# Performance work log

Hardware: AMD Instinct MI355X
Metric: run time of the kernel (lower is better)

## Reference

```python
import jax, jax.numpy as jnp
import numpy as np

N = 8192
F_IN = 256
F_OUT = 64
ALPHA = 0.2  # leaky relu negative slope
MASK_VAL = -9e15


def setup_inputs() -> dict:
    key = jax.random.key(0)
    k1, k2, k3, k4, k5, k6 = jax.random.split(key, 6)
    stdv_lin = 1.0 / np.sqrt(F_IN)
    stdv_a = 1.0 / np.sqrt(2 * F_OUT)
    return {
        "input": jax.random.normal(k1, (N, F_IN), dtype=jnp.float32),
        "adj": jax.random.randint(k2, (N, N), 0, 2, dtype=jnp.int32),
        "W": jax.random.uniform(k3, (F_IN, F_OUT), minval=-stdv_lin, maxval=stdv_lin, dtype=jnp.float32),
        "b_lin": jax.random.uniform(k4, (F_OUT,), minval=-stdv_lin, maxval=stdv_lin, dtype=jnp.float32),
        "a": jax.random.uniform(k5, (2 * F_OUT, 1), minval=-stdv_a, maxval=stdv_a, dtype=jnp.float32),
        "bias": jax.random.uniform(k6, (F_OUT,), minval=-stdv_a, maxval=stdv_a, dtype=jnp.float32),
    }


def reference(input, adj, W, b_lin, a, bias):
    # h = Linear(input): [N, F_OUT]
    h = input @ W + b_lin
    # e[i,j] = leaky_relu(a1 . h_i + a2 . h_j)  (equivalent to the repeat/cat/matmul in torch,
    # without materializing the [N, N, 2*F_OUT] tensor)
    a1 = a[:F_OUT, 0]
    a2 = a[F_OUT:, 0]
    s1 = h @ a1  # [N]
    s2 = h @ a2  # [N]
    e = jax.nn.leaky_relu(s1[:, None] + s2[None, :], negative_slope=ALPHA)  # [N, N]
    attention = jnp.where(adj > 0, e, MASK_VAL)
    attention = jax.nn.softmax(attention, axis=1)
    # dropout is identity in eval mode (training=False)
    output = attention @ h + bias
    return output
```

## Files before the change

### kernel.cpp

```cpp
#include <hip/hip_runtime.h>

#define N 8192
#define FIN 256
#define FOUT 64
#define ALPHA 0.2f

typedef float f32x4 __attribute__((ext_vector_type(4)));
typedef short s16x4 __attribute__((ext_vector_type(4)));

static __device__ __forceinline__ unsigned short f2bf(float x) {
    unsigned u = __float_as_uint(x);
    u += 0x7fffu + ((u >> 16) & 1u);
    return (unsigned short)(u >> 16);
}

__global__ __launch_bounds__(256) void k_linear(
    const float* __restrict__ input, const float* __restrict__ W,
    const float* __restrict__ b_lin, const float* __restrict__ a,
    unsigned short* __restrict__ hT, float* __restrict__ s1, float* __restrict__ s2)
{
    __shared__ float in_sh[32 * FIN];
    __shared__ float hst[64][33];
    int t = threadIdx.x;
    int i0 = blockIdx.x * 32;

    const float4* gin = (const float4*)(input + (size_t)i0 * FIN);
    float4* lin = (float4*)in_sh;
#pragma unroll
    for (int m = 0; m < 8; m++) lin[m * 256 + t] = gin[m * 256 + t];

    int f = t & 63, g = t >> 6;
    float a1v = a[f], a2v = a[FOUT + f], blv = b_lin[f];
    __syncthreads();

    float h[8];
#pragma unroll
    for (int r = 0; r < 8; r++) h[r] = blv;
#pragma unroll 4
    for (int k = 0; k < FIN; k++) {
        float wv = W[k * FOUT + f];
#pragma unroll
        for (int r = 0; r < 8; r++) h[r] += in_sh[(g * 8 + r) * FIN + k] * wv;
    }

#pragma unroll
    for (int r = 0; r < 8; r++) {
        hst[f][g * 8 + r] = h[r];
        float v1 = h[r] * a1v, v2 = h[r] * a2v;
#pragma unroll
        for (int d = 1; d < 64; d <<= 1) { v1 += __shfl_xor(v1, d); v2 += __shfl_xor(v2, d); }
        if (f == 0) { s1[i0 + g * 8 + r] = v1; s2[i0 + g * 8 + r] = v2; }
    }
    __syncthreads();

    int fo = t >> 2, seg = t & 3;
    unsigned pk[4];
#pragma unroll
    for (int m = 0; m < 4; m++) {
        unsigned lo = f2bf(hst[fo][seg * 8 + 2 * m]);
        unsigned hi = f2bf(hst[fo][seg * 8 + 2 * m + 1]);
        pk[m] = lo | (hi << 16);
    }
    int4 v; v.x = (int)pk[0]; v.y = (int)pk[1]; v.z = (int)pk[2]; v.w = (int)pk[3];
    *(int4*)(hT + (size_t)fo * N + i0 + seg * 8) = v;
}

__global__ __launch_bounds__(256) void k_s2max(const float* __restrict__ s2,
                                               float* __restrict__ s2max)
{
    __shared__ float red[4];
    int t = threadIdx.x;
    float m = -1e30f;
    for (int k = t; k < N; k += 256) m = fmaxf(m, s2[k]);
#pragma unroll
    for (int d = 1; d < 64; d <<= 1) m = fmaxf(m, __shfl_xor(m, d));
    if ((t & 63) == 0) red[t >> 6] = m;
    __syncthreads();
    if (t == 0) s2max[0] = fmaxf(fmaxf(red[0], red[1]), fmaxf(red[2], red[3]));
}

__global__ __launch_bounds__(256) void k_attn(
    const int* __restrict__ adj, const float* __restrict__ s1g,
    const float* __restrict__ s2g, const unsigned short* __restrict__ hT,
    const float* __restrict__ s2maxp, const float* __restrict__ bias,
    float* __restrict__ numP, float* __restrict__ denP, float* __restrict__ out,
    int log2c)
{
    extern __shared__ char smem[];
    unsigned short* tile = (unsigned short*)smem;
    int clen = N >> log2c;
    float* s2sh = (float*)(smem + 9216);
    float* densh = (float*)(smem + 9216 + (clen << 2));

    const float LOG2E = 1.4426950408889634f;
    int bid = blockIdx.x;
    int chunk = bid & ((1 << log2c) - 1);
    int rb = bid >> log2c;
    int jstart = chunk * clen;
    int t = threadIdx.x, w = t >> 6, l = t & 63;
    int l15 = l & 15, kg = l >> 4;

    for (int idx = t; idx < (clen >> 2); idx += 256)
        ((float4*)s2sh)[idx] = ((const float4*)(s2g + jstart))[idx];

    int i0 = rb * 64;
    int i = i0 + w * 16 + l15;
    float s1v = s1g[i];
    float s2m = s2maxp[0];
    float mx = s1v + s2m; mx = fmaxf(mx, ALPHA * mx);
    float m2 = mx * LOG2E;

    f32x4 acc[4] = {};
    float dacc = 0.f;
    const int4* adjrow = (const int4*)(adj + (size_t)i * N);
    __syncthreads();

    int iters = clen >> 6;
    for (int it = 0; it < iters; it++) {
        int j0 = it * 64;
#pragma unroll
        for (int m = 0; m < 2; m++) {
            int c = t + m * 256;
            int fr = c >> 3, off = (c & 7) * 8;
            *(int4*)(tile + fr * 72 + off) =
                *(const int4*)(hT + (size_t)fr * N + jstart + j0 + off);
        }
        s16x4 afr[4];
#pragma unroll
        for (int kb = 0; kb < 4; kb++) {
            int jloc = j0 + kb * 16 + kg * 4;
            int4 av = adjrow[(jstart + jloc) >> 2];
            float4 sv = *(const float4*)&s2sh[jloc];
            float p0, p1, p2, p3;
            { float x = s1v + sv.x; x = fmaxf(x, ALPHA * x); p0 = (av.x > 0) ? exp2f(x * LOG2E - m2) : 0.f; }
            { float x = s1v + sv.y; x = fmaxf(x, ALPHA * x); p1 = (av.y > 0) ? exp2f(x * LOG2E - m2) : 0.f; }
            { float x = s1v + sv.z; x = fmaxf(x, ALPHA * x); p2 = (av.z > 0) ? exp2f(x * LOG2E - m2) : 0.f; }
            { float x = s1v + sv.w; x = fmaxf(x, ALPHA * x); p3 = (av.w > 0) ? exp2f(x * LOG2E - m2) : 0.f; }
            dacc += (p0 + p1) + (p2 + p3);
            s16x4 af;
            af[0] = (short)f2bf(p0); af[1] = (short)f2bf(p1);
            af[2] = (short)f2bf(p2); af[3] = (short)f2bf(p3);
            afr[kb] = af;
        }
        __syncthreads();
#pragma unroll
        for (int nt = 0; nt < 4; nt++) {
#pragma unroll
            for (int kb = 0; kb < 4; kb++) {
                s16x4 bfr = *(const s16x4*)(tile + (nt * 16 + l15) * 72 + kb * 16 + kg * 4);
                acc[nt] = __builtin_amdgcn_mfma_f32_16x16x16bf16_1k(afr[kb], bfr, acc[nt], 0, 0, 0);
            }
        }
        __syncthreads();
    }

    dacc += __shfl_xor(dacc, 16);
    dacc += __shfl_xor(dacc, 32);

    if (log2c == 0) {
        if (l < 16) densh[w * 16 + l] = dacc;
        __syncthreads();
#pragma unroll
        for (int nt = 0; nt < 4; nt++) {
#pragma unroll
            for (int r = 0; r < 4; r++) {
                int orow = w * 16 + kg * 4 + r;
                out[(size_t)(i0 + orow) * FOUT + nt * 16 + l15] =
                    acc[nt][r] / densh[orow] + bias[nt * 16 + l15];
            }
        }
    } else {
        if (l < 16) denP[(size_t)chunk * N + i0 + w * 16 + l] = dacc;
#pragma unroll
        for (int nt = 0; nt < 4; nt++) {
#pragma unroll
            for (int r = 0; r < 4; r++) {
                int orow = w * 16 + kg * 4 + r;
                numP[((size_t)chunk * N + i0 + orow) * FOUT + nt * 16 + l15] = acc[nt][r];
            }
        }
    }
}

__global__ __launch_bounds__(256) void k_finalize(
    const float* __restrict__ numP, const float* __restrict__ denP,
    const float* __restrict__ bias, float* __restrict__ out, int chunks)
{
    int idx = blockIdx.x * 256 + threadIdx.x;
    int i = idx >> 6, f = idx & 63;
    float nsum = 0.f, dsum = 0.f;
    for (int c = 0; c < chunks; c++) {
        nsum += numP[(size_t)c * (N * FOUT) + idx];
        dsum += denP[(size_t)c * N + i];
    }
    out[idx] = nsum / dsum + bias[f];
}

extern "C" void kernel_launch(void* const* d_in, const int* in_sizes, int n_in,
                              void* d_out, int out_size, void* d_ws, size_t ws_size,
                              hipStream_t stream)
{
    const float* input = (const float*)d_in[0];
    const int*   adj   = (const int*)d_in[1];
    const float* W     = (const float*)d_in[2];
    const float* b_lin = (const float*)d_in[3];
    const float* a     = (const float*)d_in[4];
    const float* bias  = (const float*)d_in[5];
    float* out = (float*)d_out;

    char* ws = (char*)d_ws;
    unsigned short* hT = (unsigned short*)ws;
    float* s1    = (float*)(ws + 1048576);
    float* s2    = (float*)(ws + 1048576 + 32768);
    float* s2max = (float*)(ws + 1048576 + 65536);
    size_t fixed = 1048576 + 65536 + 256;

    int log2c = 3;
    while (log2c > 0) {
        size_t need = (((size_t)N * FOUT + N) * 4u) << log2c;
        if (fixed + need <= ws_size) break;
        log2c--;
    }
    float* numP = (float*)(ws + fixed);
    float* denP = (float*)(ws + fixed + (((size_t)N * FOUT * 4) << log2c));

    hipLaunchKernelGGL(k_linear, dim3(256), dim3(256), 0, stream,
                       input, W, b_lin, a, hT, s1, s2);
    hipLaunchKernelGGL(k_s2max, dim3(1), dim3(256), 0, stream, s2, s2max);

    int clen = N >> log2c;
    size_t smem = 9216 + ((size_t)clen << 2) + 256;
    hipLaunchKernelGGL(k_attn, dim3(128 << log2c), dim3(256), smem, stream,
                       adj, s1, s2, hT, s2max, bias, numP, denP, out, log2c);
    if (log2c > 0)
        hipLaunchKernelGGL(k_finalize, dim3(2048), dim3(256), 0, stream,
                           numP, denP, bias, out, 1 << log2c);
}
```

Measured before the change: 94.73 us.

## Pre-swizzle h into MFMA fragment layout, prefetch adj, fuse s2 max via atomics

The linear kernel now writes h in a blocked bf16 layout that matches the MFMA B-fragment order. The attention kernel can then load B operands straight from global memory, with no LDS tile staging and no __syncthreads per iteration. Adjacency rows are register double-buffered so the next tile's loads are issued before the current exp/MFMA work. The separate s2-max kernel is replaced by an order-preserving atomicMax inside k_linear, which now runs smaller 16-row blocks, with a memset to initialise the key. The cost is more global and L2 traffic for B fragments, which each wave re-reads, and higher register pressure from the prefetch buffers.

Measured after the change: 129.3 us. 1.36x slower.

```diff
diff --git a/kernel.cpp b/kernel.cpp
--- a/kernel.cpp
+++ b/kernel.cpp
@@ -17,80 +17,76 @@
 __global__ __launch_bounds__(256) void k_linear(
     const float* __restrict__ input, const float* __restrict__ W,
     const float* __restrict__ b_lin, const float* __restrict__ a,
-    unsigned short* __restrict__ hT, float* __restrict__ s1, float* __restrict__ s2)
-{
-    __shared__ float in_sh[32 * FIN];
-    __shared__ float hst[64][33];
-    int t = threadIdx.x;
-    int i0 = blockIdx.x * 32;
-
-    const float4* gin = (const float4*)(input + (size_t)i0 * FIN);
-    float4* lin = (float4*)in_sh;
-#pragma unroll
-    for (int m = 0; m < 8; m++) lin[m * 256 + t] = gin[m * 256 + t];
-
-    int f = t & 63, g = t >> 6;
-    float a1v = a[f], a2v = a[FOUT + f], blv = b_lin[f];
+    unsigned short* __restrict__ hTf, float* __restrict__ s1, float* __restrict__ s2,
+    unsigned* __restrict__ s2max_enc)
+{
+    __shared__ float in_sh[16 * FIN];
+    __shared__ float hst[64][17];
+    int t = threadIdx.x, w = t >> 6, f = t & 63;
+    int i0 = blockIdx.x * 16;
+
+#pragma unroll
+    for (int r = 0; r < 4; r++) {
+        int row = w * 4 + r;
+        *(float4*)&in_sh[row * FIN + f * 4] =
+            *(const float4*)(input + (size_t)(i0 + row) * FIN + f * 4);
+    }
+
+    float a1v = a[f], a2v = a[FOUT + f];
+    float h[4];
+#pragma unroll
+    for (int r = 0; r < 4; r++) h[r] = b_lin[f];
+
+    for (int k4 = 0; k4 < FIN / 4; k4++) {
+        float wv0 = W[(k4 * 4 + 0) * FOUT + f];
+        float wv1 = W[(k4 * 4 + 1) * FOUT + f];
+        float wv2 = W[(k4 * 4 + 2) * FOUT + f];
+        float wv3 = W[(k4 * 4 + 3) * FOUT + f];
+#pragma unroll
+        for (int r = 0; r < 4; r++) {
+            float4 iv = *(const float4*)&in_sh[(w * 4 + r) * FIN + k4 * 4];
+            h[r] = fmaf(iv.x, wv0, h[r]);
+            h[r] = fmaf(iv.y, wv1, h[r]);
+            h[r] = fmaf(iv.z, wv2, h[r]);
+            h[r] = fmaf(iv.w, wv3, h[r]);
+        }
+    }
+
+    float wmax = -1e30f;
+#pragma unroll
+    for (int r = 0; r < 4; r++) {
+        hst[f][w * 4 + r] = h[r];
+        float v1 = h[r] * a1v, v2 = h[r] * a2v;
+#pragma unroll
+        for (int d = 1; d < 64; d <<= 1) { v1 += __shfl_xor(v1, d); v2 += __shfl_xor(v2, d); }
+        wmax = fmaxf(wmax, v2);
+        if (f == 0) { s1[i0 + w * 4 + r] = v1; s2[i0 + w * 4 + r] = v2; }
+    }
+    if (f == 0) {
+        unsigned u = __float_as_uint(wmax);
+        unsigned key = (u & 0x80000000u) ? ~u : (u | 0x80000000u);
+        atomicMax(s2max_enc, key);
+    }
     __syncthreads();
 
-    float h[8];
-#pragma unroll
-    for (int r = 0; r < 8; r++) h[r] = blv;
-#pragma unroll 4
-    for (int k = 0; k < FIN; k++) {
-        float wv = W[k * FOUT + f];
-#pragma unroll
-        for (int r = 0; r < 8; r++) h[r] += in_sh[(g * 8 + r) * FIN + k] * wv;
-    }
-
-#pragma unroll
-    for (int r = 0; r < 8; r++) {
-        hst[f][g * 8 + r] = h[r];
-        float v1 = h[r] * a1v, v2 = h[r] * a2v;
-#pragma unroll
-        for (int d = 1; d < 64; d <<= 1) { v1 += __shfl_xor(v1, d); v2 += __shfl_xor(v2, d); }
-        if (f == 0) { s1[i0 + g * 8 + r] = v1; s2[i0 + g * 8 + r] = v2; }
-    }
-    __syncthreads();
-
     int fo = t >> 2, seg = t & 3;
-    unsigned pk[4];
-#pragma unroll
-    for (int m = 0; m < 4; m++) {
-        unsigned lo = f2bf(hst[fo][seg * 8 + 2 * m]);
-        unsigned hi = f2bf(hst[fo][seg * 8 + 2 * m + 1]);
-        pk[m] = lo | (hi << 16);
-    }
-    int4 v; v.x = (int)pk[0]; v.y = (int)pk[1]; v.z = (int)pk[2]; v.w = (int)pk[3];
-    *(int4*)(hT + (size_t)fo * N + i0 + seg * 8) = v;
-}
-
-__global__ __launch_bounds__(256) void k_s2max(const float* __restrict__ s2,
-                                               float* __restrict__ s2max)
-{
-    __shared__ float red[4];
-    int t = threadIdx.x;
-    float m = -1e30f;
-    for (int k = t; k < N; k += 256) m = fmaxf(m, s2[k]);
-#pragma unroll
-    for (int d = 1; d < 64; d <<= 1) m = fmaxf(m, __shfl_xor(m, d));
-    if ((t & 63) == 0) red[t >> 6] = m;
-    __syncthreads();
-    if (t == 0) s2max[0] = fmaxf(fmaxf(red[0], red[1]), fmaxf(red[2], red[3]));
+    unsigned lo = f2bf(hst[fo][seg * 4 + 0]) | ((unsigned)f2bf(hst[fo][seg * 4 + 1]) << 16);
+    unsigned hi = f2bf(hst[fo][seg * 4 + 2]) | ((unsigned)f2bf(hst[fo][seg * 4 + 3]) << 16);
+    int2 v; v.x = (int)lo; v.y = (int)hi;
+    *(int2*)(hTf + ((size_t)blockIdx.x * 64 + fo) * 16 + seg * 4) = v;
 }
 
 __global__ __launch_bounds__(256) void k_attn(
     const int* __restrict__ adj, const float* __restrict__ s1g,
-    const float* __restrict__ s2g, const unsigned short* __restrict__ hT,
-    const float* __restrict__ s2maxp, const float* __restrict__ bias,
+    const float* __restrict__ s2g, const unsigned short* __restrict__ hTf,
+    const unsigned* __restrict__ s2max_enc, const float* __restrict__ bias,
     float* __restrict__ numP, float* __restrict__ denP, float* __restrict__ out,
     int log2c)
 {
     extern __shared__ char smem[];
-    unsigned short* tile = (unsigned short*)smem;
     int clen = N >> log2c;
-    float* s2sh = (float*)(smem + 9216);
-    float* densh = (float*)(smem + 9216 + (clen << 2));
+    float* s2sh = (float*)smem;
+    float* densh = (float*)(smem + (clen << 2));
 
     const float LOG2E = 1.4426950408889634f;
     int bid = blockIdx.x;
@@ -99,6 +95,7 @@
     int jstart = chunk * clen;
     int t = threadIdx.x, w = t >> 6, l = t & 63;
     int l15 = l & 15, kg = l >> 4;
+    int p_l = l15 * 16 + kg * 4;
 
     for (int idx = t; idx < (clen >> 2); idx += 256)
         ((float4*)s2sh)[idx] = ((const float4*)(s2g + jstart))[idx];
@@ -106,52 +103,63 @@
     int i0 = rb * 64;
     int i = i0 + w * 16 + l15;
     float s1v = s1g[i];
-    float s2m = s2maxp[0];
+    unsigned key = *s2max_enc;
+    unsigned su = (key & 0x80000000u) ? (key ^ 0x80000000u) : ~key;
+    float s2m = __uint_as_float(su);
     float mx = s1v + s2m; mx = fmaxf(mx, ALPHA * mx);
     float m2 = mx * LOG2E;
 
+    const int4* adjrow = (const int4*)(adj + (size_t)i * N);
+    int jq = jstart >> 2;
+    size_t jb0 = (size_t)(jstart >> 4);
+
+    int4 acur[4];
+#pragma unroll
+    for (int kb = 0; kb < 4; kb++) acur[kb] = adjrow[jq + kb * 4 + kg];
+
     f32x4 acc[4] = {};
     float dacc = 0.f;
-    const int4* adjrow = (const int4*)(adj + (size_t)i * N);
     __syncthreads();
 
     int iters = clen >> 6;
     for (int it = 0; it < iters; it++) {
-        int j0 = it * 64;
-#pragma unroll
-        for (int m = 0; m < 2; m++) {
-            int c = t + m * 256;
-            int fr = c >> 3, off = (c & 7) * 8;
-            *(int4*)(tile + fr * 72 + off) =
-                *(const int4*)(hT + (size_t)fr * N + jstart + j0 + off);
+        int4 anext[4];
+        if (it + 1 < iters) {
+#pragma unroll
+            for (int kb = 0; kb < 4; kb++)
+                anext[kb] = adjrow[jq + (it + 1) * 16 + kb * 4 + kg];
         }
         s16x4 afr[4];
 #pragma unroll
         for (int kb = 0; kb < 4; kb++) {
-            int jloc = j0 + kb * 16 + kg * 4;
-            int4 av = adjrow[(jstart + jloc) >> 2];
-            float4 sv = *(const float4*)&s2sh[jloc];
+            float4 sv = *(const float4*)&s2sh[it * 64 + kb * 16 + kg * 4];
+            int4 av = acur[kb];
             float p0, p1, p2, p3;
-            { float x = s1v + sv.x; x = fmaxf(x, ALPHA * x); p0 = (av.x > 0) ? exp2f(x * LOG2E - m2) : 0.f; }
-            { float x = s1v + sv.y; x = fmaxf(x, ALPHA * x); p1 = (av.y > 0) ? exp2f(x * LOG2E - m2) : 0.f; }
-            { float x = s1v + sv.z; x = fmaxf(x, ALPHA * x); p2 = (av.z > 0) ? exp2f(x * LOG2E - m2) : 0.f; }
-            { float x = s1v + sv.w; x = fmaxf(x, ALPHA * x); p3 = (av.w > 0) ? exp2f(x * LOG2E - m2) : 0.f; }
+            { float x = s1v + sv.x; x = fmaxf(x, ALPHA * x); p0 = (av.x > 0) ? exp2f(fmaf(x, LOG2E, -m2)) : 0.f; }
+            { float x = s1v + sv.y; x = fmaxf(x, ALPHA * x); p1 = (av.y > 0) ? exp2f(fmaf(x, LOG2E, -m2)) : 0.f; }
+            { float x = s1v + sv.z; x = fmaxf(x, ALPHA * x); p2 = (av.z > 0) ? exp2f(fmaf(x, LOG2E, -m2)) : 0.f; }
+            { float x = s1v + sv.w; x = fmaxf(x, ALPHA * x); p3 = (av.w > 0) ? exp2f(fmaf(x, LOG2E, -m2)) : 0.f; }
             dacc += (p0 + p1) + (p2 + p3);
             s16x4 af;
             af[0] = (short)f2bf(p0); af[1] = (short)f2bf(p1);
             af[2] = (short)f2bf(p2); af[3] = (short)f2bf(p3);
             afr[kb] = af;
         }
-        __syncthreads();
+        const unsigned short* bp = hTf + (jb0 + (size_t)it * 4) * 1024 + p_l;
 #pragma unroll
         for (int nt = 0; nt < 4; nt++) {
-#pragma unroll
-            for (int kb = 0; kb < 4; kb++) {
-                s16x4 bfr = *(const s16x4*)(tile + (nt * 16 + l15) * 72 + kb * 16 + kg * 4);
-                acc[nt] = __builtin_amdgcn_mfma_f32_16x16x16bf16_1k(afr[kb], bfr, acc[nt], 0, 0, 0);
-            }
-        }
-        __syncthreads();
+            const unsigned short* bq = bp + nt * 256;
+            s16x4 b0 = *(const s16x4*)(bq);
+            s16x4 b1 = *(const s16x4*)(bq + 1024);
+            s16x4 b2 = *(const s16x4*)(bq + 2048);
+            s16x4 b3 = *(const s16x4*)(bq + 3072);
+            acc[nt] = __builtin_amdgcn_mfma_f32_16x16x16bf16_1k(afr[0], b0, acc[nt], 0, 0, 0);
+            acc[nt] = __builtin_amdgcn_mfma_f32_16x16x16bf16_1k(afr[1], b1, acc[nt], 0, 0, 0);
+            acc[nt] = __builtin_amdgcn_mfma_f32_16x16x16bf16_1k(afr[2], b2, acc[nt], 0, 0, 0);
+            acc[nt] = __builtin_amdgcn_mfma_f32_16x16x16bf16_1k(afr[3], b3, acc[nt], 0, 0, 0);
+        }
+#pragma unroll
+        for (int kb = 0; kb < 4; kb++) acur[kb] = anext[kb];
     }
 
     dacc += __shfl_xor(dacc, 16);
@@ -209,10 +217,10 @@
     float* out = (float*)d_out;
 
     char* ws = (char*)d_ws;
-    unsigned short* hT = (unsigned short*)ws;
+    unsigned short* hTf = (unsigned short*)ws;
     float* s1    = (float*)(ws + 1048576);
     float* s2    = (float*)(ws + 1048576 + 32768);
-    float* s2max = (float*)(ws + 1048576 + 65536);
+    unsigned* s2max_enc = (unsigned*)(ws + 1048576 + 65536);
     size_t fixed = 1048576 + 65536 + 256;
 
     int log2c = 3;
@@ -224,14 +232,14 @@
     float* numP = (float*)(ws + fixed);
     float* denP = (float*)(ws + fixed + (((size_t)N * FOUT * 4) << log2c));
 
-    hipLaunchKernelGGL(k_linear, dim3(256), dim3(256), 0, stream,
-                       input, W, b_lin, a, hT, s1, s2);
-    hipLaunchKernelGGL(k_s2max, dim3(1), dim3(256), 0, stream, s2, s2max);
+    hipMemsetAsync(s2max_enc, 0, 4, stream);
+    hipLaunchKernelGGL(k_linear, dim3(512), dim3(256), 0, stream,
+                       input, W, b_lin, a, hTf, s1, s2, s2max_enc);
 
     int clen = N >> log2c;
-    size_t smem = 9216 + ((size_t)clen << 2) + 256;
+    size_t smem = ((size_t)clen << 2) + 256;
     hipLaunchKernelGGL(k_attn, dim3(128 << log2c), dim3(256), smem, stream,
-                       adj, s1, s2, hT, s2max, bias, numP, denP, out, log2c);
+                       adj, s1, s2, hTf, s2max_enc, bias, numP, denP, out, log2c);
     if (log2c > 0)
         hipLaunchKernelGGL(k_finalize, dim3(2048), dim3(256), 0, stream,
                            numP, denP, bias, out, 1 << log2c);
```
